# Performance work log

Hardware: AMD Instinct MI355X
Metric: run time of the kernel (lower is better)

Reference implementation:

```python
import jax, jax.numpy as jnp
import numpy as np

K = 3; PAD = 1; STRIDE = 1; EPS = 1e-5


def setup_inputs() -> dict:
    key = jax.random.key(0)
    k0, k1, k2 = jax.random.split(key, 3)
    B, C, H, W, O = 4, 256, 64, 64, 256
    x = jax.random.normal(k0, (B, C, H, W), jnp.float32)
    # offset conv: small random weights so offsets are nontrivial but bounded
    w_off = jax.random.normal(k1, (2 * K * K, C, K, K), jnp.float32) * 0.01
    b_off = jnp.zeros((2 * K * K,), jnp.float32)
    # kaiming normal, mode=fan_out: std = sqrt(2 / (O*K*K))
    w_def = jax.random.normal(k2, (O, C, K, K), jnp.float32) * np.float32(np.sqrt(2.0 / (O * K * K)))
    gamma = jnp.ones((O,), jnp.float32)
    beta = jnp.zeros((O,), jnp.float32)
    return {"x": x, "w_off": w_off, "b_off": b_off, "w_def": w_def, "gamma": gamma, "beta": beta}


def _bilinear_gather(x, py, px):
    """x: [B,C,H,W]; py,px: [B,K2,Ho,Wo] float sample coords.
    Returns [B,K2,Ho,Wo,C] with zero padding outside (per-corner masking,
    matching torchvision deform_conv2d)."""
    B, C, H, W = x.shape
    y0f = jnp.floor(py); x0f = jnp.floor(px)
    wy1 = py - y0f; wy0 = 1.0 - wy1
    wx1 = px - x0f; wx0 = 1.0 - wx1
    bidx = jnp.arange(B)[:, None, None, None]

    def corner(yf, xf, wgt):
        valid = (yf >= 0) & (yf <= H - 1) & (xf >= 0) & (xf <= W - 1)
        yc = jnp.clip(yf.astype(jnp.int32), 0, H - 1)
        xc = jnp.clip(xf.astype(jnp.int32), 0, W - 1)
        v = x[bidx, :, yc, xc]  # [B,K2,Ho,Wo,C] (advanced idx moves C last)
        return v * (wgt * valid)[..., None]

    return (corner(y0f, x0f, wy0 * wx0) + corner(y0f, x0f + 1.0, wy0 * wx1)
            + corner(y0f + 1.0, x0f, wy1 * wx0) + corner(y0f + 1.0, x0f + 1.0, wy1 * wx1))


def _forward(x, w_off, b_off, w_def, gamma, beta):
    B, C, H, W = x.shape
    O = w_def.shape[0]
    K2 = K * K
    # 1) offset-predicting conv
    off = jax.lax.conv_general_dilated(x, w_off, (STRIDE, STRIDE), ((PAD, PAD), (PAD, PAD)))
    off = off + b_off[None, :, None, None]
    Ho, Wo = off.shape[2], off.shape[3]
    off = off.reshape(B, K2, 2, Ho, Wo)  # pairs (dy, dx) per kernel tap
    # 2) deformable sampling locations
    ky, kx = jnp.meshgrid(jnp.arange(K, dtype=jnp.float32), jnp.arange(K, dtype=jnp.float32), indexing='ij')
    base_y = (jnp.arange(Ho, dtype=jnp.float32) * STRIDE - PAD)
    base_x = (jnp.arange(Wo, dtype=jnp.float32) * STRIDE - PAD)
    py = off[:, :, 0] + ky.reshape(K2)[None, :, None, None] + base_y[None, None, :, None]
    px = off[:, :, 1] + kx.reshape(K2)[None, :, None, None] + base_x[None, None, None, :]
    vals = _bilinear_gather(x, py, px)  # [B,K2,Ho,Wo,C]
    # 3) deform conv GEMM (bias=False)
    out = jnp.einsum('bkhwc,ock->bohw', vals, w_def.reshape(O, C, K2))
    # 4) BatchNorm (training mode: batch stats) + ReLU
    mean = out.mean(axis=(0, 2, 3))
    var = out.var(axis=(0, 2, 3))
    out = (out - mean[None, :, None, None]) * (gamma * jax.lax.rsqrt(var + EPS))[None, :, None, None]
    out = out + beta[None, :, None, None]
    return jax.nn.relu(out)


def reference(x, w_off, b_off, w_def, gamma, beta):
    return _forward(x, w_off, b_off, w_def, gamma, beta)
```

## Files before the change

### kernel.cpp

```cpp
#include <hip/hip_runtime.h>
#include <hip/hip_bf16.h>

typedef unsigned int  uint;
typedef unsigned short ushort;
typedef short bf16x8 __attribute__((ext_vector_type(8)));
typedef float f32x4  __attribute__((ext_vector_type(4)));

#define HW   4096
#define KD   2304

__device__ __forceinline__ void load_lds16(const void* g, void* l) {
    __builtin_amdgcn_global_load_lds((const __attribute__((address_space(1))) void*)g,
                                     (__attribute__((address_space(3))) void*)l, 16, 0, 0);
}
__device__ __forceinline__ float blo(uint u) { return __uint_as_float(u << 16); }
__device__ __forceinline__ float bhi(uint u) { return __uint_as_float(u & 0xffff0000u); }
__device__ __forceinline__ uint pack2(float e, float o) {
    __hip_bfloat16 he = __float2bfloat16(e), ho = __float2bfloat16(o);
    return (uint)(*(ushort*)&he) | ((uint)(*(ushort*)&ho) << 16);
}

__global__ __launch_bounds__(256) void prep_all(const float* __restrict__ x,
                                                const float* __restrict__ w_def,
                                                const float* __restrict__ w_off,
                                                uint* __restrict__ x2t,
                                                ushort* __restrict__ bt,
                                                ushort* __restrict__ bt0,
                                                float* __restrict__ stats) {
    __shared__ uint tl[32][65];
    int bid = blockIdx.x;
    int t = threadIdx.x;
    if (bid < 1024) {
        int ab  = bid & 63;
        int cpb = (bid >> 6) & 3;
        int b   = bid >> 8;
#pragma unroll
        for (int i = 0; i < 8; ++i) {
            int idx = i * 256 + t;
            int cp = idx >> 6, a = idx & 63;
            const float* p = x + ((size_t)(b * 256 + (cpb * 32 + cp) * 2)) * HW + ab * 64 + a;
            tl[cp][a] = pack2(p[0], p[HW]);
        }
        __syncthreads();
#pragma unroll
        for (int i = 0; i < 8; ++i) {
            int idx = i * 256 + t;
            int a = idx >> 5, cp = idx & 31;
            x2t[((size_t)b * 4096 + ab * 64 + a) * 128 + cpb * 32 + cp] = tl[cp][a];
        }
    } else if (bid < 3328) {
        int idx = (bid - 1024) * 256 + t;
        int c   = idx & 255;
        int tap = (idx >> 8) % 9;
        int o   = idx / KD;
        __hip_bfloat16 h = __float2bfloat16(w_def[(o * 256 + c) * 9 + tap]);
        bt[idx] = *(ushort*)&h;
    } else if (bid < 3616) {
        int idx = (bid - 3328) * 256 + t;
        int c   = idx & 255;
        int tap = (idx >> 8) % 9;
        int j   = idx / KD;
        float v = (j < 18) ? w_off[(j * 256 + c) * 9 + tap] : 0.f;
        __hip_bfloat16 h = __float2bfloat16(v);
        bt0[idx] = *(ushort*)&h;
    } else {
        float4 z = {0.f, 0.f, 0.f, 0.f};
        ((float4*)stats)[t] = z;
    }
}

__global__ __launch_bounds__(512) void gemm_off(const uint* __restrict__ x2t,
                                                const ushort* __restrict__ bt0,
                                                const float* __restrict__ b_off,
                                                float* __restrict__ off) {
    int id = blockIdx.x;
    int xcd = id & 7;
    int b = xcd >> 1, h = (xcd & 1) * 32 + (id >> 3);
    int t = threadIdx.x, wv = t >> 6, lane = t & 63;
    int mrow = lane & 15, quad = lane >> 4;
    int mq = wv & 3, nn = wv >> 2;

    __shared__ uint   lX[3 * 64 * 32];
    __shared__ ushort lB[32 * 576];

    f32x4 acc = {0.f, 0.f, 0.f, 0.f};

    for (int cb = 0; cb < 4; ++cb) {
#pragma unroll
        for (int s = 0; s < 3; ++s) {
            int q   = s * 8 + wv;
            int dy  = q >> 3;
            int y   = h + dy - 1;
            int sub = q & 7;
            int wl  = sub * 8 + (lane >> 3);
            int cps = ((lane & 7) ^ ((lane >> 3) & 7)) * 4;
            if ((unsigned)y < 64u) {
                const uint* src = x2t + ((size_t)(b * 4096 + y * 64 + wl)) * 128 + cb * 32 + cps;
                load_lds16(src, &lX[q * 256]);
            } else {
                uint4 z = {0u, 0u, 0u, 0u};
                *(uint4*)&lX[q * 256 + lane * 4] = z;
            }
        }
#pragma unroll
        for (int s = 0; s < 5; ++s) {
            int q = s * 8 + wv;
            if (q < 36) {
                int e = q * 512 + lane * 8;
                int o  = e / 576;
                int r  = e - o * 576;
                int chp = r >> 3;
                int ch  = chp ^ (o & 7);
                int tap = ch >> 3, k8 = ch & 7;
                const ushort* src = bt0 + (size_t)o * KD + tap * 256 + cb * 64 + k8 * 8;
                load_lds16(src, &lB[q * 512]);
            }
        }
        __syncthreads();

#pragma unroll
        for (int tap = 0; tap < 9; ++tap) {
            int dy = tap / 3, dx = tap % 3;
            int xx = mq * 16 + mrow + dx - 1;
            bool vx = (unsigned)xx < 64u;
            int xc = min(max(xx, 0), 63);
#pragma unroll
            for (int kb = 0; kb < 2; ++kb) {
                int cp0 = kb * 16 + quad * 4;
                uint4 ad = {0u, 0u, 0u, 0u};
                if (vx) ad = *(const uint4*)&lX[dy * 2048 + xc * 32 + (cp0 ^ ((xc & 7) * 4))];
                bf16x8 af = *(bf16x8*)&ad;
                int o = nn * 16 + mrow;
                int chs = (tap * 8 + (((kb * 4 + quad)) ^ (o & 7)));
                bf16x8 bfr = *(const bf16x8*)&lB[o * 576 + chs * 8];
                acc = __builtin_amdgcn_mfma_f32_16x16x32_bf16(af, bfr, acc, 0, 0, 0);
            }
        }
        __syncthreads();
    }
    {
        int o = nn * 16 + mrow;
        float bias = (o < 18) ? b_off[o] : 0.f;
        f32x4 v = acc;
        v.x += bias; v.y += bias; v.z += bias; v.w += bias;
        int wpos = mq * 16 + quad * 4;
        *(f32x4*)(off + ((size_t)(b * 32 + o)) * HW + h * 64 + wpos) = v;
    }
}

__global__ __attribute__((amdgpu_waves_per_eu(4, 4))) __launch_bounds__(1024)
void fused_main(const uint* __restrict__ x2t,
                const ushort* __restrict__ bt,
                const float* __restrict__ off,
                float* __restrict__ out,
                float* __restrict__ stats) {
    int id = blockIdx.x;
    int xcd = id & 7;
    int b = xcd >> 1, h = (xcd & 1) * 32 + (id >> 3);
    int t = threadIdx.x;
    int wv = t >> 6, lane = t & 63;
    int mrow = lane & 15, quad = lane >> 4;
    bool producer = (wv < 8);
    int ppos = (wv << 3) + (lane >> 3);
    int pc8  = lane & 7;
    int wvc  = wv - 8;

    __shared__ int    sAc[4][9][64];
    __shared__ float  sWc[4][9][64];
    __shared__ ushort lA[4][64 * 64];

    for (int i = t; i < 576; i += 1024) {
        int tap = i >> 6, ww = i & 63;
        int hw = h * 64 + ww;
        float oy = off[((size_t)(b * 32 + 2 * tap)) * HW + hw];
        float ox = off[((size_t)(b * 32 + 2 * tap + 1)) * HW + hw];
        float py = oy + (float)(tap / 3 + h - 1);
        float px = ox + (float)(tap % 3 + ww - 1);
        float y0f = floorf(py), x0f = floorf(px);
        float wy1 = py - y0f, wx1 = px - x0f;
        float wy0 = 1.f - wy1, wx0 = 1.f - wx1;
        bool vy0 = (y0f >= 0.f) && (y0f <= 63.f);
        bool vy1 = (y0f >= -1.f) && (y0f <= 62.f);
        bool vx0 = (x0f >= 0.f) && (x0f <= 63.f);
        bool vx1 = (x0f >= -1.f) && (x0f <= 62.f);
        int iy0 = min(max((int)y0f, 0), 63),  iy1 = min(max((int)y0f + 1, 0), 63);
        int ix0 = min(max((int)x0f, 0), 63),  ix1 = min(max((int)x0f + 1, 0), 63);
        sAc[0][tap][ww] = iy0 * 64 + ix0;
        sAc[1][tap][ww] = iy0 * 64 + ix1;
        sAc[2][tap][ww] = iy1 * 64 + ix0;
        sAc[3][tap][ww] = iy1 * 64 + ix1;
        sWc[0][tap][ww] = wy0 * wx0 * (float)(vy0 && vx0);
        sWc[1][tap][ww] = wy0 * wx1 * (float)(vy0 && vx1);
        sWc[2][tap][ww] = wy1 * wx0 * (float)(vy1 && vx0);
        sWc[3][tap][ww] = wy1 * wx1 * (float)(vy1 && vx1);
    }
    __syncthreads();

    f32x4 acc[4][2];
#pragma unroll
    for (int m = 0; m < 4; ++m)
#pragma unroll
        for (int n = 0; n < 2; ++n) acc[m][n] = {0.f, 0.f, 0.f, 0.f};

    const uint* xb = x2t + (size_t)b * 4096 * 128;

    auto issue_gathers = [&](int sl, uint4 (&g)[4]) {
        int tap = sl >> 2, cb = sl & 3;
        const uint* xp = xb + cb * 32 + pc8 * 4;
        g[0] = *(const uint4*)(xp + (size_t)sAc[0][tap][ppos] * 128);
        g[1] = *(const uint4*)(xp + (size_t)sAc[1][tap][ppos] * 128);
        g[2] = *(const uint4*)(xp + (size_t)sAc[2][tap][ppos] * 128);
        g[3] = *(const uint4*)(xp + (size_t)sAc[3][tap][ppos] * 128);
    };
    auto finish = [&](int sl, ushort* lAb, const uint4 (&g)[4]) {
        int tap = sl >> 2;
        float f0 = sWc[0][tap][ppos], f1 = sWc[1][tap][ppos];
        float f2 = sWc[2][tap][ppos], f3 = sWc[3][tap][ppos];
        const uint* c0 = (const uint*)&g[0];
        const uint* c1 = (const uint*)&g[1];
        const uint* c2 = (const uint*)&g[2];
        const uint* c3 = (const uint*)&g[3];
        uint r[4];
#pragma unroll
        for (int j = 0; j < 4; ++j) {
            float ev = f0 * blo(c0[j]) + f1 * blo(c1[j]) + f2 * blo(c2[j]) + f3 * blo(c3[j]);
            float ov = f0 * bhi(c0[j]) + f1 * bhi(c1[j]) + f2 * bhi(c2[j]) + f3 * bhi(c3[j]);
            r[j] = pack2(ev, ov);
        }
        uint4 gg = {r[0], r[1], r[2], r[3]};
        *(uint4*)&lAb[ppos * 64 + ((pc8 ^ (ppos & 7)) * 8)] = gg;
    };
    auto loadB = [&](int sl, bf16x8 (&br)[4]) {
        int tap = sl >> 2, cb = sl & 3;
        const ushort* base = bt + tap * 256 + cb * 64 + quad * 8;
#pragma unroll
        for (int kb = 0; kb < 2; ++kb)
#pragma unroll
            for (int n = 0; n < 2; ++n) {
                int r = wvc * 32 + n * 16 + mrow;
                br[kb * 2 + n] = *(const bf16x8*)(base + (size_t)r * KD + kb * 32);
            }
    };
    auto mfma_pass = [&](int bi, const bf16x8 (&br)[4]) {
#pragma unroll
        for (int kb = 0; kb < 2; ++kb) {
            bf16x8 af[4];
#pragma unroll
            for (int m = 0; m < 4; ++m) {
                int r = m * 16 + mrow;
                af[m] = *(const bf16x8*)&lA[bi][r * 64 + (((kb * 4 + quad) ^ (r & 7)) * 8)];
            }
#pragma unroll
            for (int n = 0; n < 2; ++n)
#pragma unroll
                for (int m = 0; m < 4; ++m)
                    acc[m][n] = __builtin_amdgcn_mfma_f32_16x16x32_bf16(af[m], br[kb * 2 + n], acc[m][n], 0, 0, 0);
        }
    };

    uint4 gA[4];
    bf16x8 brA[4], brB[4];
    if (producer) {
        issue_gathers(0, gA);
        finish(0, lA[0], gA);
        issue_gathers(1, gA);
        finish(1, lA[1], gA);
        asm volatile("s_waitcnt lgkmcnt(0)" ::: "memory");
    } else {
        loadB(0, brA);
        loadB(1, brB);
    }
    __builtin_amdgcn_s_barrier();
    __builtin_amdgcn_sched_barrier(0);

    for (int s = 0; s < 36; s += 2) {
        if (producer) {
            if (s + 2 < 36) {
                issue_gathers(s + 2, gA);
                finish(s + 2, lA[(s + 2) & 3], gA);
                issue_gathers(s + 3, gA);
                finish(s + 3, lA[(s + 3) & 3], gA);
                asm volatile("s_waitcnt lgkmcnt(0)" ::: "memory");
            }
        } else {
            __builtin_amdgcn_s_setprio(1);
            mfma_pass(s & 3, brA);
            mfma_pass((s + 1) & 3, brB);
            __builtin_amdgcn_s_setprio(0);
            if (s + 2 < 36) loadB(s + 2, brA);
            if (s + 3 < 36) loadB(s + 3, brB);
        }
        __builtin_amdgcn_s_barrier();
        __builtin_amdgcn_sched_barrier(0);
    }

    if (!producer) {
#pragma unroll
        for (int n = 0; n < 2; ++n) {
            int o = wvc * 32 + n * 16 + mrow;
            float ss = 0.f, qq = 0.f;
#pragma unroll
            for (int m = 0; m < 4; ++m) {
                int pos = m * 16 + quad * 4;
                f32x4 v = acc[m][n];
                *(f32x4*)(out + ((size_t)(b * 256 + o)) * HW + h * 64 + pos) = v;
                ss += v.x + v.y + v.z + v.w;
                qq += v.x * v.x + v.y * v.y + v.z * v.z + v.w * v.w;
            }
            ss += __shfl_xor(ss, 16); ss += __shfl_xor(ss, 32);
            qq += __shfl_xor(qq, 16); qq += __shfl_xor(qq, 32);
            if (quad == 0) {
                atomicAdd(&stats[o], ss);
                atomicAdd(&stats[512 + o], qq);
            }
        }
    }
}

__global__ __launch_bounds__(256) void bn_apply(float* __restrict__ out,
                                                const float* __restrict__ stats,
                                                const float* __restrict__ gamma,
                                                const float* __restrict__ beta) {
    int bid = blockIdx.x;
    int o = (bid >> 2) & 255;
    float S = stats[o], S2 = stats[512 + o];
    float mu  = S * (1.f / 16384.f);
    float var = S2 * (1.f / 16384.f) - mu * mu;
    float sc  = gamma[o] * rsqrtf(var + 1e-5f);
    float be  = beta[o];
    int idx4 = bid * 256 + threadIdx.x;
    float4 v = ((const float4*)out)[idx4];
    v.x = fmaxf((v.x - mu) * sc + be, 0.f);
    v.y = fmaxf((v.y - mu) * sc + be, 0.f);
    v.z = fmaxf((v.z - mu) * sc + be, 0.f);
    v.w = fmaxf((v.w - mu) * sc + be, 0.f);
    ((float4*)out)[idx4] = v;
}

extern "C" void kernel_launch(void* const* d_in, const int* in_sizes, int n_in,
                              void* d_out, int out_size, void* d_ws, size_t ws_size,
                              hipStream_t stream) {
    const float* x     = (const float*)d_in[0];
    const float* w_off = (const float*)d_in[1];
    const float* b_off = (const float*)d_in[2];
    const float* w_def = (const float*)d_in[3];
    const float* gamma = (const float*)d_in[4];
    const float* beta  = (const float*)d_in[5];
    float* out = (float*)d_out;

    char* ws = (char*)d_ws;
    uint*   x2t   = (uint*)ws;
    ushort* bt    = (ushort*)(ws + 8388608);
    ushort* bt0   = (ushort*)(ws + 9568256);
    float*  off   = (float*)(ws + 9715712);
    float*  stats = (float*)(ws + 11812864);

    prep_all  <<<3617, 256, 0, stream>>>(x, w_def, w_off, x2t, bt, bt0, stats);
    gemm_off  <<<256, 512, 0, stream>>>(x2t, bt0, b_off, off);
    fused_main<<<256, 1024, 0, stream>>>(x2t, bt, off, out, stats);
    bn_apply  <<<4096, 256, 0, stream>>>(out, stats, gamma, beta);
}
```

Before: 148.6 us.

## Fuse offset-conv GEMM into main deformable kernel via shared-memory offsets

Removes the separate gemm_off kernel and computes the per-row offset convolution inside fused_main's prologue. The eight producer waves run the MFMAs while all 16 waves cooperatively stage the tiles, and the offsets are written to shared memory instead of a global buffer. Shared memory is now a manually aliased byte array so the offset-stage buffers overlap the later gather buffers. This saves one kernel launch and the global round trip of the offset tensor, but serialises the offset GEMM at the start of each main block, with half the waves idle during it.

```diff
diff --git a/kernel.cpp b/kernel.cpp
--- a/kernel.cpp
+++ b/kernel.cpp
@@ -69,89 +69,11 @@
     }
 }
 
-__global__ __launch_bounds__(512) void gemm_off(const uint* __restrict__ x2t,
-                                                const ushort* __restrict__ bt0,
-                                                const float* __restrict__ b_off,
-                                                float* __restrict__ off) {
-    int id = blockIdx.x;
-    int xcd = id & 7;
-    int b = xcd >> 1, h = (xcd & 1) * 32 + (id >> 3);
-    int t = threadIdx.x, wv = t >> 6, lane = t & 63;
-    int mrow = lane & 15, quad = lane >> 4;
-    int mq = wv & 3, nn = wv >> 2;
-
-    __shared__ uint   lX[3 * 64 * 32];
-    __shared__ ushort lB[32 * 576];
-
-    f32x4 acc = {0.f, 0.f, 0.f, 0.f};
-
-    for (int cb = 0; cb < 4; ++cb) {
-#pragma unroll
-        for (int s = 0; s < 3; ++s) {
-            int q   = s * 8 + wv;
-            int dy  = q >> 3;
-            int y   = h + dy - 1;
-            int sub = q & 7;
-            int wl  = sub * 8 + (lane >> 3);
-            int cps = ((lane & 7) ^ ((lane >> 3) & 7)) * 4;
-            if ((unsigned)y < 64u) {
-                const uint* src = x2t + ((size_t)(b * 4096 + y * 64 + wl)) * 128 + cb * 32 + cps;
-                load_lds16(src, &lX[q * 256]);
-            } else {
-                uint4 z = {0u, 0u, 0u, 0u};
-                *(uint4*)&lX[q * 256 + lane * 4] = z;
-            }
-        }
-#pragma unroll
-        for (int s = 0; s < 5; ++s) {
-            int q = s * 8 + wv;
-            if (q < 36) {
-                int e = q * 512 + lane * 8;
-                int o  = e / 576;
-                int r  = e - o * 576;
-                int chp = r >> 3;
-                int ch  = chp ^ (o & 7);
-                int tap = ch >> 3, k8 = ch & 7;
-                const ushort* src = bt0 + (size_t)o * KD + tap * 256 + cb * 64 + k8 * 8;
-                load_lds16(src, &lB[q * 512]);
-            }
-        }
-        __syncthreads();
-
-#pragma unroll
-        for (int tap = 0; tap < 9; ++tap) {
-            int dy = tap / 3, dx = tap % 3;
-            int xx = mq * 16 + mrow + dx - 1;
-            bool vx = (unsigned)xx < 64u;
-            int xc = min(max(xx, 0), 63);
-#pragma unroll
-            for (int kb = 0; kb < 2; ++kb) {
-                int cp0 = kb * 16 + quad * 4;
-                uint4 ad = {0u, 0u, 0u, 0u};
-                if (vx) ad = *(const uint4*)&lX[dy * 2048 + xc * 32 + (cp0 ^ ((xc & 7) * 4))];
-                bf16x8 af = *(bf16x8*)&ad;
-                int o = nn * 16 + mrow;
-                int chs = (tap * 8 + (((kb * 4 + quad)) ^ (o & 7)));
-                bf16x8 bfr = *(const bf16x8*)&lB[o * 576 + chs * 8];
-                acc = __builtin_amdgcn_mfma_f32_16x16x32_bf16(af, bfr, acc, 0, 0, 0);
-            }
-        }
-        __syncthreads();
-    }
-    {
-        int o = nn * 16 + mrow;
-        float bias = (o < 18) ? b_off[o] : 0.f;
-        f32x4 v = acc;
-        v.x += bias; v.y += bias; v.z += bias; v.w += bias;
-        int wpos = mq * 16 + quad * 4;
-        *(f32x4*)(off + ((size_t)(b * 32 + o)) * HW + h * 64 + wpos) = v;
-    }
-}
-
 __global__ __attribute__((amdgpu_waves_per_eu(4, 4))) __launch_bounds__(1024)
 void fused_main(const uint* __restrict__ x2t,
                 const ushort* __restrict__ bt,
-                const float* __restrict__ off,
+                const ushort* __restrict__ bt0,
+                const float* __restrict__ b_off,
                 float* __restrict__ out,
                 float* __restrict__ stats) {
     int id = blockIdx.x;
@@ -165,15 +87,91 @@
     int pc8  = lane & 7;
     int wvc  = wv - 8;
 
-    __shared__ int    sAc[4][9][64];
-    __shared__ float  sWc[4][9][64];
-    __shared__ ushort lA[4][64 * 64];
+    __shared__ __align__(16) char smem[66048];
+    uint*   lX   = (uint*)smem;
+    ushort* lB0  = (ushort*)(smem + 24576);
+    float*  sOff = (float*)(smem + 61440);
+    int*    sAc  = (int*)smem;
+    float*  sWc  = (float*)(smem + 9216);
+    ushort* lA   = (ushort*)(smem + 18432);
+
+    {
+        f32x4 accO = {0.f, 0.f, 0.f, 0.f};
+        int mq = wv & 3, nn = (wv >> 2) & 1;
+        for (int cb = 0; cb < 4; ++cb) {
+#pragma unroll
+            for (int s = 0; s < 2; ++s) {
+                int q = s * 16 + wv;
+                if (q < 24) {
+                    int dy  = q >> 3;
+                    int y   = h + dy - 1;
+                    int sub = q & 7;
+                    int wl  = sub * 8 + (lane >> 3);
+                    int cps = ((lane & 7) ^ ((lane >> 3) & 7)) * 4;
+                    if ((unsigned)y < 64u) {
+                        const uint* src = x2t + ((size_t)(b * 4096 + y * 64 + wl)) * 128 + cb * 32 + cps;
+                        load_lds16(src, &lX[q * 256]);
+                    } else {
+                        uint4 z = {0u, 0u, 0u, 0u};
+                        *(uint4*)&lX[q * 256 + lane * 4] = z;
+                    }
+                }
+            }
+#pragma unroll
+            for (int s = 0; s < 3; ++s) {
+                int q = s * 16 + wv;
+                if (q < 36) {
+                    int e = q * 512 + lane * 8;
+                    int o  = e / 576;
+                    int r  = e - o * 576;
+                    int chp = r >> 3;
+                    int ch  = chp ^ (o & 7);
+                    int tap = ch >> 3, k8 = ch & 7;
+                    const ushort* src = bt0 + (size_t)o * KD + tap * 256 + cb * 64 + k8 * 8;
+                    load_lds16(src, &lB0[q * 512]);
+                }
+            }
+            __syncthreads();
+            if (producer) {
+#pragma unroll
+                for (int tap = 0; tap < 9; ++tap) {
+                    int dy = tap / 3, dx = tap % 3;
+                    int xx = mq * 16 + mrow + dx - 1;
+                    bool vx = (unsigned)xx < 64u;
+                    int xc = min(max(xx, 0), 63);
+#pragma unroll
+                    for (int kb = 0; kb < 2; ++kb) {
+                        int cp0 = kb * 16 + quad * 4;
+                        uint4 ad = {0u, 0u, 0u, 0u};
+                        if (vx) ad = *(const uint4*)&lX[dy * 2048 + xc * 32 + (cp0 ^ ((xc & 7) * 4))];
+                        bf16x8 af = *(bf16x8*)&ad;
+                        int o = nn * 16 + mrow;
+                        int chs = (tap * 8 + (((kb * 4 + quad)) ^ (o & 7)));
+                        bf16x8 bfr = *(const bf16x8*)&lB0[o * 576 + chs * 8];
+                        accO = __builtin_amdgcn_mfma_f32_16x16x32_bf16(af, bfr, accO, 0, 0, 0);
+                    }
+                }
+            }
+            __syncthreads();
+        }
+        if (producer) {
+            int o = nn * 16 + mrow;
+            if (o < 18) {
+                float bias = b_off[o];
+                int wpos = mq * 16 + quad * 4;
+                sOff[o * 64 + wpos + 0] = accO.x + bias;
+                sOff[o * 64 + wpos + 1] = accO.y + bias;
+                sOff[o * 64 + wpos + 2] = accO.z + bias;
+                sOff[o * 64 + wpos + 3] = accO.w + bias;
+            }
+        }
+        __syncthreads();
+    }
 
     for (int i = t; i < 576; i += 1024) {
         int tap = i >> 6, ww = i & 63;
-        int hw = h * 64 + ww;
-        float oy = off[((size_t)(b * 32 + 2 * tap)) * HW + hw];
-        float ox = off[((size_t)(b * 32 + 2 * tap + 1)) * HW + hw];
+        float oy = sOff[(2 * tap) * 64 + ww];
+        float ox = sOff[(2 * tap + 1) * 64 + ww];
         float py = oy + (float)(tap / 3 + h - 1);
         float px = ox + (float)(tap % 3 + ww - 1);
         float y0f = floorf(py), x0f = floorf(px);
@@ -185,14 +183,14 @@
         bool vx1 = (x0f >= -1.f) && (x0f <= 62.f);
         int iy0 = min(max((int)y0f, 0), 63),  iy1 = min(max((int)y0f + 1, 0), 63);
         int ix0 = min(max((int)x0f, 0), 63),  ix1 = min(max((int)x0f + 1, 0), 63);
-        sAc[0][tap][ww] = iy0 * 64 + ix0;
-        sAc[1][tap][ww] = iy0 * 64 + ix1;
-        sAc[2][tap][ww] = iy1 * 64 + ix0;
-        sAc[3][tap][ww] = iy1 * 64 + ix1;
-        sWc[0][tap][ww] = wy0 * wx0 * (float)(vy0 && vx0);
-        sWc[1][tap][ww] = wy0 * wx1 * (float)(vy0 && vx1);
-        sWc[2][tap][ww] = wy1 * wx0 * (float)(vy1 && vx0);
-        sWc[3][tap][ww] = wy1 * wx1 * (float)(vy1 && vx1);
+        sAc[0 * 576 + tap * 64 + ww] = iy0 * 64 + ix0;
+        sAc[1 * 576 + tap * 64 + ww] = iy0 * 64 + ix1;
+        sAc[2 * 576 + tap * 64 + ww] = iy1 * 64 + ix0;
+        sAc[3 * 576 + tap * 64 + ww] = iy1 * 64 + ix1;
+        sWc[0 * 576 + tap * 64 + ww] = wy0 * wx0 * (float)(vy0 && vx0);
+        sWc[1 * 576 + tap * 64 + ww] = wy0 * wx1 * (float)(vy0 && vx1);
+        sWc[2 * 576 + tap * 64 + ww] = wy1 * wx0 * (float)(vy1 && vx0);
+        sWc[3 * 576 + tap * 64 + ww] = wy1 * wx1 * (float)(vy1 && vx1);
     }
     __syncthreads();
 
@@ -207,15 +205,15 @@
     auto issue_gathers = [&](int sl, uint4 (&g)[4]) {
         int tap = sl >> 2, cb = sl & 3;
         const uint* xp = xb + cb * 32 + pc8 * 4;
-        g[0] = *(const uint4*)(xp + (size_t)sAc[0][tap][ppos] * 128);
-        g[1] = *(const uint4*)(xp + (size_t)sAc[1][tap][ppos] * 128);
-        g[2] = *(const uint4*)(xp + (size_t)sAc[2][tap][ppos] * 128);
-        g[3] = *(const uint4*)(xp + (size_t)sAc[3][tap][ppos] * 128);
+        g[0] = *(const uint4*)(xp + (size_t)sAc[0 * 576 + tap * 64 + ppos] * 128);
+        g[1] = *(const uint4*)(xp + (size_t)sAc[1 * 576 + tap * 64 + ppos] * 128);
+        g[2] = *(const uint4*)(xp + (size_t)sAc[2 * 576 + tap * 64 + ppos] * 128);
+        g[3] = *(const uint4*)(xp + (size_t)sAc[3 * 576 + tap * 64 + ppos] * 128);
     };
     auto finish = [&](int sl, ushort* lAb, const uint4 (&g)[4]) {
         int tap = sl >> 2;
-        float f0 = sWc[0][tap][ppos], f1 = sWc[1][tap][ppos];
-        float f2 = sWc[2][tap][ppos], f3 = sWc[3][tap][ppos];
+        float f0 = sWc[0 * 576 + tap * 64 + ppos], f1 = sWc[1 * 576 + tap * 64 + ppos];
+        float f2 = sWc[2 * 576 + tap * 64 + ppos], f3 = sWc[3 * 576 + tap * 64 + ppos];
         const uint* c0 = (const uint*)&g[0];
         const uint* c1 = (const uint*)&g[1];
         const uint* c2 = (const uint*)&g[2];
@@ -248,7 +246,7 @@
 #pragma unroll
             for (int m = 0; m < 4; ++m) {
                 int r = m * 16 + mrow;
-                af[m] = *(const bf16x8*)&lA[bi][r * 64 + (((kb * 4 + quad) ^ (r & 7)) * 8)];
+                af[m] = *(const bf16x8*)&lA[bi * 4096 + r * 64 + (((kb * 4 + quad) ^ (r & 7)) * 8)];
             }
 #pragma unroll
             for (int n = 0; n < 2; ++n)
@@ -262,9 +260,9 @@
     bf16x8 brA[4], brB[4];
     if (producer) {
         issue_gathers(0, gA);
-        finish(0, lA[0], gA);
+        finish(0, &lA[0], gA);
         issue_gathers(1, gA);
-        finish(1, lA[1], gA);
+        finish(1, &lA[4096], gA);
         asm volatile("s_waitcnt lgkmcnt(0)" ::: "memory");
     } else {
         loadB(0, brA);
@@ -277,9 +275,9 @@
         if (producer) {
             if (s + 2 < 36) {
                 issue_gathers(s + 2, gA);
-                finish(s + 2, lA[(s + 2) & 3], gA);
+                finish(s + 2, &lA[((s + 2) & 3) * 4096], gA);
                 issue_gathers(s + 3, gA);
-                finish(s + 3, lA[(s + 3) & 3], gA);
+                finish(s + 3, &lA[((s + 3) & 3) * 4096], gA);
                 asm volatile("s_waitcnt lgkmcnt(0)" ::: "memory");
             }
         } else {
@@ -352,11 +350,9 @@
     uint*   x2t   = (uint*)ws;
     ushort* bt    = (ushort*)(ws + 8388608);
     ushort* bt0   = (ushort*)(ws + 9568256);
-    float*  off   = (float*)(ws + 9715712);
-    float*  stats = (float*)(ws + 11812864);
+    float*  stats = (float*)(ws + 9715712);
 
     prep_all  <<<3617, 256, 0, stream>>>(x, w_def, w_off, x2t, bt, bt0, stats);
-    gemm_off  <<<256, 512, 0, stream>>>(x2t, bt0, b_off, off);
-    fused_main<<<256, 1024, 0, stream>>>(x2t, bt, off, out, stats);
+    fused_main<<<256, 1024, 0, stream>>>(x2t, bt, bt0, b_off, out, stats);
     bn_apply  <<<4096, 256, 0, stream>>>(out, stats, gamma, beta);
 }
```

New measurement: 144.6 us. 1.03x faster.
